# Kernel optimization log

Hardware: AMD Instinct MI355X
Metric: run time of the kernel (lower is better)

The kernel has to match this reference:

```python
import jax, jax.numpy as jnp
import numpy as np

N_STROKES = 512
H = 256
W = 256
EPS = 1e-6


def setup_inputs() -> dict:
    key = jax.random.key(0)
    k1, k2, k3, k4, k5, k6 = jax.random.split(key, 6)
    canvas = jnp.zeros((3, H, W), dtype=jnp.float32)
    target = jax.random.uniform(k1, (3, H, W), dtype=jnp.float32)
    offset = jax.random.normal(k2, (N_STROKES, 2, 1), dtype=jnp.float32) * 0.5 + 0.5
    sigma = jax.random.uniform(k3, (N_STROKES, 2, 1), dtype=jnp.float32) * 0.5 + 0.2
    theta = jax.random.uniform(k4, (N_STROKES, 1), dtype=jnp.float32) * (2.0 * np.pi)
    color = jax.random.uniform(k5, (N_STROKES, 3, 1, 1), dtype=jnp.float32)
    alpha = jax.random.normal(k6, (N_STROKES, 1, 1, 1), dtype=jnp.float32) * 0.1
    return {"canvas": canvas, "target": target, "offset": offset,
            "sigma": sigma, "theta": theta, "color": color, "alpha": alpha}


def reference(canvas, target, offset, sigma, theta, color, alpha):
    h, w = canvas.shape[-2:]
    ratio = w / h  # width_to_height_ratio

    # normalized pixel grid, matching torch.linspace(0, w-1, w)/w
    ws = jnp.arange(w, dtype=jnp.float32) / w
    hs = jnp.arange(h, dtype=jnp.float32) / h
    x, y = jnp.meshgrid(ws, hs, indexing="xy")          # (H, W) each
    coords = jnp.stack([x, y], axis=0).reshape(1, 2, -1)  # (1, 2, H*W)
    coords = coords - offset                              # (n, 2, H*W)

    # rotation matrix per stroke: [[cos, -sin], [sin, -cos]] (as in source)
    cos_t = jnp.cos(theta)
    sin_t = jnp.sin(theta)
    rot = jnp.concatenate([cos_t, -sin_t, sin_t, -cos_t], axis=-1).reshape(-1, 2, 2)
    coords = jnp.einsum("nij,njp->nip", rot, coords)      # (n, 2, H*W)

    # aspect-corrected sigma (only for the gaussian field, not the loss)
    sig = jnp.concatenate([sigma[:, :1] / ratio, sigma[:, 1:]], axis=1)  # (n, 2, 1)

    quad = jnp.sum(jnp.square(coords) / (2.0 * jnp.square(sig)), axis=1)  # (n, H*W)
    pdf = jnp.exp(-quad)
    maxes = jnp.max(pdf, axis=-1, keepdims=True)          # per-stroke max-normalize
    pdf = pdf / (maxes + EPS)

    strokes = pdf.reshape(-1, 1, h, w) * alpha * color    # (n, 3, H, W)
    out = jax.nn.sigmoid(canvas + jnp.sum(strokes, axis=0))

    # loss_fn(out, target)
    l2 = jnp.mean(jnp.square(out - target))
    sharpness = jnp.mean(jnp.abs(1.0 - sigma[:, 0] / sigma[:, 1])) * 0.001
    transparency = -jnp.mean(jnp.abs(alpha)) * 0.001
    mse = jnp.mean(jnp.square(target - out))
    psnr = 10.0 * jnp.log10(1.0 / (mse + 1e-12))
    loss = l2 + transparency + sharpness - psnr / 30.0
    return out, loss
```

## Files before the change

kernel.cpp:

```cpp
#include <hip/hip_runtime.h>
#include <hip/hip_bf16.h>

#define HH 256
#define WW 256
#define NPIX (HH*WW)
#define NS 512
#define PSTRIDE 12
#define L2_SLOT   (NS*PSTRIDE)
#define CNT_SLOT  (NS*PSTRIDE + 1)

#define TEAMS 8
#define SPT   (NS/TEAMS)
#define PPT   4
#define BLK   512
#define K2_GRID 256

#define L2E 1.4426950408889634f

#if __has_builtin(__builtin_amdgcn_exp2f)
#define EXP2F(x) __builtin_amdgcn_exp2f(x)
#else
#define EXP2F(x) exp2f(x)
#endif
#if __has_builtin(__builtin_amdgcn_rcpf)
#define RCPF(x) __builtin_amdgcn_rcpf(x)
#else
#define RCPF(x) (1.0f/(x))
#endif

__global__ __launch_bounds__(256) void k1_prep(
    const float* __restrict__ offset, const float* __restrict__ sigma,
    const float* __restrict__ theta,  const float* __restrict__ color,
    const float* __restrict__ alpha,  float* __restrict__ wsf)
{
    const int n = blockIdx.x;
    const int i = threadIdx.x;

    const float ox = offset[2*n], oy = offset[2*n+1];
    const float s0 = sigma[2*n],  s1 = sigma[2*n+1];
    const float th = theta[n];

    const float kk = sqrtf(0.5f * L2E);
    const float ra = kk / s0;
    const float rb = kk / s1;

    float s, c;
    __sincosf(th, &s, &c);
    const float P = ra * c,  Q = -ra * s,  T1 = ra * (-c * ox + s * oy);
    const float R = rb * s,  S = -rb * c,  T2 = rb * (-s * ox + c * oy);

    const float y     = (float)i / (float)HH;
    const float beta  = fmaf(Q, y, T1);
    const float delta = fmaf(S, y, T2);
    const float A     = P * P + R * R;
    const float xstar = -(P * beta + R * delta) / A;
    int j0 = (int)floorf(xstar * (float)WW);
    j0 = max(0, min(WW - 1, j0));
    const int j1 = min(WW - 1, j0 + 1);
    const float x0 = (float)j0 / (float)WW, x1 = (float)j1 / (float)WW;
    const float u0 = fmaf(P, x0, beta),  v0 = fmaf(R, x0, delta);
    const float u1 = fmaf(P, x1, beta),  v1 = fmaf(R, x1, delta);
    float q = fminf(u0*u0 + v0*v0, u1*u1 + v1*v1);

    #pragma unroll
    for (int off = 32; off > 0; off >>= 1)
        q = fminf(q, __shfl_down(q, off));
    __shared__ float wmin[4];
    if ((i & 63) == 0) wmin[i >> 6] = q;
    __syncthreads();

    if (i == 0) {
        const float qmin   = fminf(fminf(wmin[0], wmin[1]), fminf(wmin[2], wmin[3]));
        const float maxpdf = EXP2F(-qmin);
        const float base   = alpha[n] / (maxpdf + 1e-6f);
        float* p = wsf + n * PSTRIDE;
        p[0] = P;  p[1] = Q;  p[2] = T1;
        p[3] = R;  p[4] = S;  p[5] = T2;
        p[6] = base * color[3*n];
        p[7] = base * color[3*n+1];
        p[8] = base * color[3*n+2];
        p[9]  = fabsf(1.0f - s0 / s1);
        p[10] = fabsf(alpha[n]);
        p[11] = 0.0f;
        if (n == 0) {
            wsf[L2_SLOT] = 0.0f;
            ((int*)wsf)[CNT_SLOT] = 0;
        }
    }
}

__global__ __launch_bounds__(512) void k2_paint(
    const float* __restrict__ canvas, const float* __restrict__ target,
    const float* __restrict__ prm,    float* __restrict__ out,
    float* __restrict__ l2acc,        int* __restrict__ cnt)
{
    const int tid  = threadIdx.x;
    const int t    = tid & 63;
    const int team = __builtin_amdgcn_readfirstlane(tid >> 6);
    const int row  = blockIdx.x;
    const float y  = (float)row * (1.0f / (float)HH);

    float xk[PPT];
    #pragma unroll
    for (int k = 0; k < PPT; ++k) xk[k] = (float)(t + 64*k) * (1.0f / (float)WW);

    const float* __restrict__ tp = prm + team * (SPT * PSTRIDE);

    float acc[PPT][3] = {};
    #pragma unroll 2
    for (int n = 0; n < SPT; ++n) {
        const float* sp = tp + n * PSTRIDE;
        const float P  = sp[0], Q  = sp[1], T1 = sp[2];
        const float R  = sp[3], S  = sp[4], T2 = sp[5];
        const float c0 = sp[6], c1 = sp[7], c2 = sp[8];
        const float beta  = fmaf(Q, y, T1);
        const float delta = fmaf(S, y, T2);
        #pragma unroll
        for (int k = 0; k < PPT; ++k) {
            const float U = fmaf(P, xk[k], beta);
            const float V = fmaf(R, xk[k], delta);
            const float e = EXP2F(-fmaf(U, U, V * V));
            acc[k][0] = fmaf(e, c0, acc[k][0]);
            acc[k][1] = fmaf(e, c1, acc[k][1]);
            acc[k][2] = fmaf(e, c2, acc[k][2]);
        }
    }

    __shared__ float sacc[TEAMS][WW][3];
    #pragma unroll
    for (int k = 0; k < PPT; ++k) {
        sacc[team][t + 64*k][0] = acc[k][0];
        sacc[team][t + 64*k][1] = acc[k][1];
        sacc[team][t + 64*k][2] = acc[k][2];
    }
    __syncthreads();

    __shared__ float lw[4];
    __shared__ int sdone;
    if (tid < WW) {
        float z0 = 0.0f, z1 = 0.0f, z2 = 0.0f;
        #pragma unroll
        for (int tm = 0; tm < TEAMS; ++tm) {
            z0 += sacc[tm][tid][0];
            z1 += sacc[tm][tid][1];
            z2 += sacc[tm][tid][2];
        }
        const int p = row * WW + tid;
        z0 += canvas[p];
        z1 += canvas[NPIX + p];
        z2 += canvas[2*NPIX + p];
        const float o0 = RCPF(1.0f + EXP2F(-z0 * L2E));
        const float o1 = RCPF(1.0f + EXP2F(-z1 * L2E));
        const float o2 = RCPF(1.0f + EXP2F(-z2 * L2E));
        out[p]          = o0;
        out[NPIX + p]   = o1;
        out[2*NPIX + p] = o2;
        const float d0 = o0 - target[p];
        const float d1 = o1 - target[NPIX + p];
        const float d2 = o2 - target[2*NPIX + p];
        float l2loc = d0*d0 + d1*d1 + d2*d2;
        #pragma unroll
        for (int off = 32; off > 0; off >>= 1)
            l2loc += __shfl_down(l2loc, off);
        if (t == 0) lw[tid >> 6] = l2loc;
    }
    __syncthreads();

    if (tid == 0) {
        atomicAdd(l2acc, lw[0] + lw[1] + lw[2] + lw[3]);
        __threadfence();
        const int old = atomicAdd(cnt, 1);
        sdone = (old == K2_GRID - 1) ? 1 : 0;
    }
    __syncthreads();

    if (sdone) {
        float sh = prm[tid * PSTRIDE + 9];
        float tr = prm[tid * PSTRIDE + 10];
        #pragma unroll
        for (int off = 32; off > 0; off >>= 1) {
            sh += __shfl_down(sh, off);
            tr += __shfl_down(tr, off);
        }
        if (t == 0) { sacc[0][tid >> 6][0] = sh; sacc[0][tid >> 6][1] = tr; }
        __syncthreads();
        if (tid == 0) {
            float shs = 0.0f, trs = 0.0f;
            #pragma unroll
            for (int w = 0; w < TEAMS; ++w) { shs += sacc[0][w][0]; trs += sacc[0][w][1]; }
            const float l2tot  = atomicAdd(l2acc, 0.0f);
            const float l2     = l2tot / (float)(3 * NPIX);
            const float sharp  = (shs / (float)NS) * 0.001f;
            const float transp = -(trs / (float)NS) * 0.001f;
            const float psnr   = 10.0f * log10f(1.0f / (l2 + 1e-12f));
            out[3 * NPIX] = l2 + transp + sharp - psnr / 30.0f;
        }
    }
}

extern "C" void kernel_launch(void* const* d_in, const int* in_sizes, int n_in,
                              void* d_out, int out_size, void* d_ws, size_t ws_size,
                              hipStream_t stream)
{
    const float* canvas = (const float*)d_in[0];
    const float* target = (const float*)d_in[1];
    const float* offset = (const float*)d_in[2];
    const float* sigma  = (const float*)d_in[3];
    const float* theta  = (const float*)d_in[4];
    const float* color  = (const float*)d_in[5];
    const float* alpha  = (const float*)d_in[6];
    float* out = (float*)d_out;
    float* wsf = (float*)d_ws;

    k1_prep<<<NS, 256, 0, stream>>>(offset, sigma, theta, color, alpha, wsf);
    k2_paint<<<K2_GRID, BLK, 0, stream>>>(canvas, target, wsf, out,
                                          wsf + L2_SLOT, (int*)wsf + CNT_SLOT);
}
```

Measured before the change: 91.19 us.

## Fuse stroke prep into paint kernel and replace per-pixel exp with recurrence

Result: faster. 84.64 us (-7.2%).

```diff
diff --git a/kernel.cpp b/kernel.cpp
--- a/kernel.cpp
+++ b/kernel.cpp
@@ -5,17 +5,14 @@
 #define WW 256
 #define NPIX (HH*WW)
 #define NS 512
-#define PSTRIDE 12
-#define L2_SLOT   (NS*PSTRIDE)
-#define CNT_SLOT  (NS*PSTRIDE + 1)
 
 #define TEAMS 8
 #define SPT   (NS/TEAMS)
-#define PPT   4
 #define BLK   512
 #define K2_GRID 256
 
-#define L2E 1.4426950408889634f
+#define L2E  1.4426950408889634f
+#define XMAX (255.0f/256.0f)
 
 #if __has_builtin(__builtin_amdgcn_exp2f)
 #define EXP2F(x) __builtin_amdgcn_exp2f(x)
@@ -28,111 +25,149 @@
 #define RCPF(x) (1.0f/(x))
 #endif
 
-__global__ __launch_bounds__(256) void k1_prep(
+__device__ __forceinline__ float rlane(float v, int l) {
+#if __has_builtin(__builtin_amdgcn_readlane)
+    return __int_as_float(__builtin_amdgcn_readlane(__float_as_int(v), l));
+#else
+    return __shfl(v, l, 64);
+#endif
+}
+
+__global__ __launch_bounds__(64) void k0_init(float* __restrict__ wsf)
+{
+    if (threadIdx.x == 0) { wsf[0] = 0.0f; ((int*)wsf)[1] = 0; }
+}
+
+__global__ __launch_bounds__(512) void k2_paint(
+    const float* __restrict__ canvas, const float* __restrict__ target,
     const float* __restrict__ offset, const float* __restrict__ sigma,
     const float* __restrict__ theta,  const float* __restrict__ color,
-    const float* __restrict__ alpha,  float* __restrict__ wsf)
+    const float* __restrict__ alpha,  float* __restrict__ out,
+    float* __restrict__ l2acc,        int* __restrict__ cnt)
 {
-    const int n = blockIdx.x;
-    const int i = threadIdx.x;
-
-    const float ox = offset[2*n], oy = offset[2*n+1];
-    const float s0 = sigma[2*n],  s1 = sigma[2*n+1];
-    const float th = theta[n];
-
-    const float kk = sqrtf(0.5f * L2E);
+    const int tid = threadIdx.x;
+    const int t   = tid & 63;
+    const int w   = tid >> 6;
+    const int row = blockIdx.x;
+    const float y = (float)row * (1.0f / 256.0f);
+
+    const int m = tid;
+    const float ox = offset[2*m], oy = offset[2*m+1];
+    const float s0 = sigma[2*m],  s1 = sigma[2*m+1];
+    const float th = theta[m];
+    const float al = alpha[m];
+
+    const float kk = 0.84932180028802f;
     const float ra = kk / s0;
     const float rb = kk / s1;
-
-    float s, c;
-    __sincosf(th, &s, &c);
-    const float P = ra * c,  Q = -ra * s,  T1 = ra * (-c * ox + s * oy);
-    const float R = rb * s,  S = -rb * c,  T2 = rb * (-s * ox + c * oy);
-
-    const float y     = (float)i / (float)HH;
-    const float beta  = fmaf(Q, y, T1);
-    const float delta = fmaf(S, y, T2);
-    const float A     = P * P + R * R;
-    const float xstar = -(P * beta + R * delta) / A;
-    int j0 = (int)floorf(xstar * (float)WW);
-    j0 = max(0, min(WW - 1, j0));
-    const int j1 = min(WW - 1, j0 + 1);
-    const float x0 = (float)j0 / (float)WW, x1 = (float)j1 / (float)WW;
-    const float u0 = fmaf(P, x0, beta),  v0 = fmaf(R, x0, delta);
-    const float u1 = fmaf(P, x1, beta),  v1 = fmaf(R, x1, delta);
-    float q = fminf(u0*u0 + v0*v0, u1*u1 + v1*v1);
+    float sn, cs;
+    __sincosf(th, &sn, &cs);
+    const float P = ra * cs,  Q = -ra * sn,  T1 = ra * (-cs * ox + sn * oy);
+    const float R = rb * sn,  S = -rb * cs,  T2 = rb * (-sn * ox + cs * oy);
+
+    const float den_x = P*P + R*R;
+    const float den_y = Q*Q + S*S;
+    float bx = 0.0f, by = 0.0f, qb = 3.0e38f;
+    {
+        const float det = P*S - Q*R;
+        if (fabsf(det) > 1e-5f) {
+            const float xc = (Q*T2 - S*T1) / det;
+            const float yc = (R*T1 - P*T2) / det;
+            if (xc >= 0.0f && xc <= XMAX && yc >= 0.0f && yc <= XMAX) {
+                const float u = fmaf(P, xc, fmaf(Q, yc, T1));
+                const float v = fmaf(R, xc, fmaf(S, yc, T2));
+                const float qq = u*u + v*v;
+                if (qq < qb) { qb = qq; bx = xc; by = yc; }
+            }
+        }
+        #pragma unroll
+        for (int e = 0; e < 2; ++e) {
+            const float X = e ? XMAX : 0.0f;
+            const float be = fmaf(P, X, T1), de = fmaf(R, X, T2);
+            float ye = -(Q*be + S*de) / den_y;
+            ye = fminf(fmaxf(ye, 0.0f), XMAX);
+            const float u = fmaf(Q, ye, be), v = fmaf(S, ye, de);
+            const float qq = u*u + v*v;
+            if (qq < qb) { qb = qq; bx = X; by = ye; }
+        }
+        #pragma unroll
+        for (int e = 0; e < 2; ++e) {
+            const float Y = e ? XMAX : 0.0f;
+            const float ae = fmaf(Q, Y, T1), ge = fmaf(S, Y, T2);
+            float xe = -(P*ae + R*ge) / den_x;
+            xe = fminf(fmaxf(xe, 0.0f), XMAX);
+            const float u = fmaf(P, xe, ae), v = fmaf(R, xe, ge);
+            const float qq = u*u + v*v;
+            if (qq < qb) { qb = qq; bx = xe; by = Y; }
+        }
+    }
+    float qmin = 3.0e38f;
+    {
+        const int jr = (int)floorf(fmaf(bx, 256.0f, 0.5f));
+        const int ir = (int)floorf(fmaf(by, 256.0f, 0.5f));
+        #pragma unroll
+        for (int di = -1; di <= 1; ++di) {
+            const int ii = min(255, max(0, ir + di));
+            const float yg = (float)ii * (1.0f / 256.0f);
+            const float bg = fmaf(Q, yg, T1), dg = fmaf(S, yg, T2);
+            #pragma unroll
+            for (int dj = -1; dj <= 1; ++dj) {
+                const int jj = min(255, max(0, jr + dj));
+                const float xg = (float)jj * (1.0f / 256.0f);
+                const float u = fmaf(P, xg, bg), v = fmaf(R, xg, dg);
+                qmin = fminf(qmin, u*u + v*v);
+            }
+        }
+    }
+    const float maxpdf = EXP2F(-qmin);
+    const float base   = al / (maxpdf + 1e-6f);
+    const float rk0 = base * color[3*m];
+    const float rk1 = base * color[3*m+1];
+    const float rk2 = base * color[3*m+2];
+    const float shv = fabsf(1.0f - s0 / s1);
+    const float trv = fabsf(al);
+
+    const float by_ = fmaf(Q, y, T1);
+    const float dy_ = fmaf(S, y, T2);
+    const float na2 = -den_x;
+    const float na1 = -2.0f * (P * by_ + R * dy_);
+    const float na0 = -(by_ * by_ + dy_ * dy_);
+    const float rtd = 0.5f * na2;
+    const float rcd = fmaf(na2, 0.0625f, 0.25f * na1);
+    const float rEf = EXP2F(0.125f * na2);
+
+    const float x0 = (float)t * (1.0f / 256.0f);
+    float a00=0,a01=0,a02=0, a10=0,a11=0,a12=0, a20=0,a21=0,a22=0, a30=0,a31=0,a32=0;
 
     #pragma unroll
-    for (int off = 32; off > 0; off >>= 1)
-        q = fminf(q, __shfl_down(q, off));
-    __shared__ float wmin[4];
-    if ((i & 63) == 0) wmin[i >> 6] = q;
-    __syncthreads();
-
-    if (i == 0) {
-        const float qmin   = fminf(fminf(wmin[0], wmin[1]), fminf(wmin[2], wmin[3]));
-        const float maxpdf = EXP2F(-qmin);
-        const float base   = alpha[n] / (maxpdf + 1e-6f);
-        float* p = wsf + n * PSTRIDE;
-        p[0] = P;  p[1] = Q;  p[2] = T1;
-        p[3] = R;  p[4] = S;  p[5] = T2;
-        p[6] = base * color[3*n];
-        p[7] = base * color[3*n+1];
-        p[8] = base * color[3*n+2];
-        p[9]  = fabsf(1.0f - s0 / s1);
-        p[10] = fabsf(alpha[n]);
-        p[11] = 0.0f;
-        if (n == 0) {
-            wsf[L2_SLOT] = 0.0f;
-            ((int*)wsf)[CNT_SLOT] = 0;
-        }
-    }
-}
-
-__global__ __launch_bounds__(512) void k2_paint(
-    const float* __restrict__ canvas, const float* __restrict__ target,
-    const float* __restrict__ prm,    float* __restrict__ out,
-    float* __restrict__ l2acc,        int* __restrict__ cnt)
-{
-    const int tid  = threadIdx.x;
-    const int t    = tid & 63;
-    const int team = __builtin_amdgcn_readfirstlane(tid >> 6);
-    const int row  = blockIdx.x;
-    const float y  = (float)row * (1.0f / (float)HH);
-
-    float xk[PPT];
-    #pragma unroll
-    for (int k = 0; k < PPT; ++k) xk[k] = (float)(t + 64*k) * (1.0f / (float)WW);
-
-    const float* __restrict__ tp = prm + team * (SPT * PSTRIDE);
-
-    float acc[PPT][3] = {};
-    #pragma unroll 2
     for (int n = 0; n < SPT; ++n) {
-        const float* sp = tp + n * PSTRIDE;
-        const float P  = sp[0], Q  = sp[1], T1 = sp[2];
-        const float R  = sp[3], S  = sp[4], T2 = sp[5];
-        const float c0 = sp[6], c1 = sp[7], c2 = sp[8];
-        const float beta  = fmaf(Q, y, T1);
-        const float delta = fmaf(S, y, T2);
-        #pragma unroll
-        for (int k = 0; k < PPT; ++k) {
-            const float U = fmaf(P, xk[k], beta);
-            const float V = fmaf(R, xk[k], delta);
-            const float e = EXP2F(-fmaf(U, U, V * V));
-            acc[k][0] = fmaf(e, c0, acc[k][0]);
-            acc[k][1] = fmaf(e, c1, acc[k][1]);
-            acc[k][2] = fmaf(e, c2, acc[k][2]);
-        }
+        const float c2 = rlane(na2, n);
+        const float c1 = rlane(na1, n);
+        const float c0 = rlane(na0, n);
+        const float td = rlane(rtd, n);
+        const float cd = rlane(rcd, n);
+        const float Ef = rlane(rEf, n);
+        const float k0 = rlane(rk0, n);
+        const float k1 = rlane(rk1, n);
+        const float k2 = rlane(rk2, n);
+        const float g0 = fmaf(fmaf(c2, x0, c1), x0, c0);
+        const float d0 = fminf(fmaf(td, x0, cd), 120.0f);
+        float G = EXP2F(g0);
+        float D = EXP2F(d0);
+        a00 = fmaf(G, k0, a00); a01 = fmaf(G, k1, a01); a02 = fmaf(G, k2, a02);
+        G *= D; D *= Ef;
+        a10 = fmaf(G, k0, a10); a11 = fmaf(G, k1, a11); a12 = fmaf(G, k2, a12);
+        G *= D; D *= Ef;
+        a20 = fmaf(G, k0, a20); a21 = fmaf(G, k1, a21); a22 = fmaf(G, k2, a22);
+        G *= D;
+        a30 = fmaf(G, k0, a30); a31 = fmaf(G, k1, a31); a32 = fmaf(G, k2, a32);
     }
 
     __shared__ float sacc[TEAMS][WW][3];
-    #pragma unroll
-    for (int k = 0; k < PPT; ++k) {
-        sacc[team][t + 64*k][0] = acc[k][0];
-        sacc[team][t + 64*k][1] = acc[k][1];
-        sacc[team][t + 64*k][2] = acc[k][2];
-    }
+    sacc[w][t      ][0] = a00; sacc[w][t      ][1] = a01; sacc[w][t      ][2] = a02;
+    sacc[w][t +  64][0] = a10; sacc[w][t +  64][1] = a11; sacc[w][t +  64][2] = a12;
+    sacc[w][t + 128][0] = a20; sacc[w][t + 128][1] = a21; sacc[w][t + 128][2] = a22;
+    sacc[w][t + 192][0] = a30; sacc[w][t + 192][1] = a31; sacc[w][t + 192][2] = a32;
     __syncthreads();
 
     __shared__ float lw[4];
@@ -175,19 +210,18 @@
     __syncthreads();
 
     if (sdone) {
-        float sh = prm[tid * PSTRIDE + 9];
-        float tr = prm[tid * PSTRIDE + 10];
+        float sh = shv, tr = trv;
         #pragma unroll
         for (int off = 32; off > 0; off >>= 1) {
             sh += __shfl_down(sh, off);
             tr += __shfl_down(tr, off);
         }
-        if (t == 0) { sacc[0][tid >> 6][0] = sh; sacc[0][tid >> 6][1] = tr; }
+        if (t == 0) { sacc[0][w][0] = sh; sacc[0][w][1] = tr; }
         __syncthreads();
         if (tid == 0) {
             float shs = 0.0f, trs = 0.0f;
             #pragma unroll
-            for (int w = 0; w < TEAMS; ++w) { shs += sacc[0][w][0]; trs += sacc[0][w][1]; }
+            for (int v = 0; v < TEAMS; ++v) { shs += sacc[0][v][0]; trs += sacc[0][v][1]; }
             const float l2tot  = atomicAdd(l2acc, 0.0f);
             const float l2     = l2tot / (float)(3 * NPIX);
             const float sharp  = (shs / (float)NS) * 0.001f;
@@ -212,7 +246,7 @@
     float* out = (float*)d_out;
     float* wsf = (float*)d_ws;
 
-    k1_prep<<<NS, 256, 0, stream>>>(offset, sigma, theta, color, alpha, wsf);
-    k2_paint<<<K2_GRID, BLK, 0, stream>>>(canvas, target, wsf, out,
-                                          wsf + L2_SLOT, (int*)wsf + CNT_SLOT);
-}
+    k0_init<<<1, 64, 0, stream>>>(wsf);
+    k2_paint<<<K2_GRID, BLK, 0, stream>>>(canvas, target, offset, sigma, theta,
+                                          color, alpha, out, wsf, (int*)wsf + 1);
+}
```
